# Optimization experiments

Hardware: AMD Instinct MI355X
Metric: run time of the kernel (lower is better)

The kernel has to match this reference:

```python
import jax, jax.numpy as jnp
import numpy as np

DIM = 768
HEADS = 12
HEAD_DIM = DIM // HEADS
SCALE = HEAD_DIM ** -0.5


def setup_inputs() -> dict:
    key = jax.random.key(0)
    ks = jax.random.split(key, 6)
    B, N = 4, 2048
    x = jax.random.normal(ks[0], (B, N, DIM), dtype=jnp.float32)
    s = DIM ** -0.5
    Wq = jax.random.normal(ks[1], (DIM, DIM), dtype=jnp.float32) * s
    Wk = jax.random.normal(ks[2], (DIM, DIM), dtype=jnp.float32) * s
    Wv = jax.random.normal(ks[3], (DIM, DIM), dtype=jnp.float32) * s
    Wp = jax.random.normal(ks[4], (DIM, DIM), dtype=jnp.float32) * s
    bp = jnp.zeros((DIM,), dtype=jnp.float32)
    return {"x": x, "Wq": Wq, "Wk": Wk, "Wv": Wv, "Wp": Wp, "bp": bp}


def reference(x, Wq, Wk, Wv, Wp, bp):
    B, N, C = x.shape
    # separate Q/K/V linears (no bias, qkv_bias=False); torch Linear: x @ W.T
    q = (x @ Wq.T).reshape(B, N, HEADS, HEAD_DIM).transpose(0, 2, 1, 3)
    k = (x @ Wk.T).reshape(B, N, HEADS, HEAD_DIM).transpose(0, 2, 1, 3)
    v = (x @ Wv.T).reshape(B, N, HEADS, HEAD_DIM).transpose(0, 2, 1, 3)
    # explicit full [B,H,N,N] attention matrix, as in the source
    attn = jnp.einsum("bhqd,bhkd->bhqk", q, k) * SCALE
    attn = jax.nn.softmax(attn, axis=-1)
    out = jnp.einsum("bhqk,bhkd->bhqd", attn, v)
    out = out.transpose(0, 2, 1, 3).reshape(B, N, C)
    return out @ Wp.T + bp
```

## Files before the change

kernel.cpp:

```cpp
#include <hip/hip_runtime.h>
#include <cstdint>

#define DIM   768
#define HEADS 12
#define HDIM  64
#define BATCH 4
#define SEQ   2048
#define MROWS (BATCH*SEQ)

typedef __bf16 bf16;
typedef __bf16 bf16x4_t __attribute__((ext_vector_type(4)));
typedef __bf16 bf16x8_t __attribute__((ext_vector_type(8)));
typedef float  f32x4_t  __attribute__((ext_vector_type(4)));
typedef short  short4_t __attribute__((ext_vector_type(4)));

__device__ __forceinline__ f32x4_t mfma16x16x16bf16(bf16x4_t a, bf16x4_t b, f32x4_t c) {
#if __has_builtin(__builtin_amdgcn_mfma_f32_16x16x16_bf16)
    return __builtin_amdgcn_mfma_f32_16x16x16_bf16(a, b, c, 0, 0, 0);
#elif __has_builtin(__builtin_amdgcn_mfma_f32_16x16x16bf16_1k)
    union U { bf16x4_t h; short4_t s; };
    U ua, ub; ua.h = a; ub.h = b;
    return __builtin_amdgcn_mfma_f32_16x16x16bf16_1k(ua.s, ub.s, c, 0, 0, 0);
#else
    asm("v_mfma_f32_16x16x16_bf16 %0, %1, %2, %0" : "+v"(c) : "v"(a), "v"(b));
    return c;
#endif
}

__global__ void cast_bf16_kernel(const float* __restrict__ src, bf16* __restrict__ dst, int n4) {
    int i = blockIdx.x * blockDim.x + threadIdx.x;
    if (i >= n4) return;
    const float4 v = reinterpret_cast<const float4*>(src)[i];
    bf16x4_t o;
    o[0] = (bf16)v.x; o[1] = (bf16)v.y; o[2] = (bf16)v.z; o[3] = (bf16)v.w;
    reinterpret_cast<bf16x4_t*>(dst)[i] = o;
}

__global__ void cast_w4_kernel(const float* __restrict__ s0, const float* __restrict__ s1,
                               const float* __restrict__ s2, const float* __restrict__ s3,
                               bf16* __restrict__ d0, bf16* __restrict__ d1,
                               bf16* __restrict__ d2, bf16* __restrict__ d3, int n4) {
    int i = blockIdx.x * blockDim.x + threadIdx.x;
    if (i >= n4) return;
    int y = blockIdx.y;
    const float* src = (y == 0) ? s0 : (y == 1) ? s1 : (y == 2) ? s2 : s3;
    bf16* dst        = (y == 0) ? d0 : (y == 1) ? d1 : (y == 2) ? d2 : d3;
    const float4 v = reinterpret_cast<const float4*>(src)[i];
    bf16x4_t o;
    o[0] = (bf16)v.x; o[1] = (bf16)v.y; o[2] = (bf16)v.z; o[3] = (bf16)v.w;
    reinterpret_cast<bf16x4_t*>(dst)[i] = o;
}

__device__ __forceinline__ void gload_lds16(const bf16* g, bf16* l) {
    __builtin_amdgcn_global_load_lds((const __attribute__((address_space(1))) void*)g,
                                     (__attribute__((address_space(3))) void*)l, 16, 0, 0);
}

__global__ __launch_bounds__(256, 2) void qkv_gemm(
        const bf16* __restrict__ X,
        const bf16* __restrict__ Wq, const bf16* __restrict__ Wk, const bf16* __restrict__ Wv,
        bf16* __restrict__ Q, bf16* __restrict__ Kd, bf16* __restrict__ Vt)
{
    __shared__ bf16 As[128*32];
    __shared__ bf16 Bs[128*32];
    const int tid  = threadIdx.x;
    const int z    = blockIdx.z;
    const bf16* W  = (z == 0) ? Wq : (z == 1 ? Wk : Wv);
    const int n0   = blockIdx.x * 128;
    const int m0   = blockIdx.y * 128;
    const int lane = tid & 63;
    const int w    = tid >> 6;
    const int wm   = (w & 1) * 64, wn = (w >> 1) * 64;
    const int lr   = lane & 15, quad = lane >> 4;

    f32x4_t acc[4][4] = {};

    for (int kk = 0; kk < DIM; kk += 32) {
        #pragma unroll
        for (int i = 0; i < 2; ++i) {
            int c = tid + i * 256;
            int row = c >> 2, ko = (c & 3) * 8;
            gload_lds16(X + (size_t)(m0 + row) * DIM + kk + ko, &As[row * 32 + ko]);
            gload_lds16(W + (size_t)(n0 + row) * DIM + kk + ko, &Bs[row * 32 + ko]);
        }
        __syncthreads();
        bf16x8_t af[4], bfr[4];
        #pragma unroll
        for (int i = 0; i < 4; ++i)
            af[i] = *reinterpret_cast<const bf16x8_t*>(&As[(wm + i * 16 + lr) * 32 + quad * 8]);
        #pragma unroll
        for (int j = 0; j < 4; ++j)
            bfr[j] = *reinterpret_cast<const bf16x8_t*>(&Bs[(wn + j * 16 + lr) * 32 + quad * 8]);
        #pragma unroll
        for (int i = 0; i < 4; ++i)
            #pragma unroll
            for (int j = 0; j < 4; ++j)
                acc[i][j] = __builtin_amdgcn_mfma_f32_16x16x32_bf16(af[i], bfr[j], acc[i][j], 0, 0, 0);
        __syncthreads();
    }

    #pragma unroll
    for (int i = 0; i < 4; ++i) {
        int mbase = m0 + wm + i * 16 + quad * 4;
        #pragma unroll
        for (int j = 0; j < 4; ++j) {
            int n = n0 + wn + j * 16 + lr;
            int h = n >> 6, d = n & 63;
            #pragma unroll
            for (int r = 0; r < 4; ++r) {
                int m = mbase + r;
                int b = m >> 11, row = m & 2047;
                bf16 v = (bf16)acc[i][j][r];
                if (z < 2) {
                    bf16* dst = (z == 0) ? Q : Kd;
                    dst[(((size_t)b * HEADS + h) * SEQ + row) * HDIM + d] = v;
                } else {
                    Vt[(((size_t)b * HEADS + h) * HDIM + d) * SEQ + row] = v;
                }
            }
        }
    }
}

__global__ __launch_bounds__(256, 2) void out_gemm(
        const bf16* __restrict__ A,
        const bf16* __restrict__ W,
        const float* __restrict__ bias,
        float* __restrict__ out)
{
    __shared__ bf16 As[128*32];
    __shared__ bf16 Bs[128*32];
    const int tid  = threadIdx.x;
    const int n0   = blockIdx.x * 128;
    const int m0   = blockIdx.y * 128;
    const int lane = tid & 63;
    const int w    = tid >> 6;
    const int wm   = (w & 1) * 64, wn = (w >> 1) * 64;
    const int lr   = lane & 15, quad = lane >> 4;

    f32x4_t acc[4][4] = {};

    for (int kk = 0; kk < DIM; kk += 32) {
        #pragma unroll
        for (int i = 0; i < 2; ++i) {
            int c = tid + i * 256;
            int row = c >> 2, ko = (c & 3) * 8;
            gload_lds16(A + (size_t)(m0 + row) * DIM + kk + ko, &As[row * 32 + ko]);
            gload_lds16(W + (size_t)(n0 + row) * DIM + kk + ko, &Bs[row * 32 + ko]);
        }
        __syncthreads();
        bf16x8_t af[4], bfr[4];
        #pragma unroll
        for (int i = 0; i < 4; ++i)
            af[i] = *reinterpret_cast<const bf16x8_t*>(&As[(wm + i * 16 + lr) * 32 + quad * 8]);
        #pragma unroll
        for (int j = 0; j < 4; ++j)
            bfr[j] = *reinterpret_cast<const bf16x8_t*>(&Bs[(wn + j * 16 + lr) * 32 + quad * 8]);
        #pragma unroll
        for (int i = 0; i < 4; ++i)
            #pragma unroll
            for (int j = 0; j < 4; ++j)
                acc[i][j] = __builtin_amdgcn_mfma_f32_16x16x32_bf16(af[i], bfr[j], acc[i][j], 0, 0, 0);
        __syncthreads();
    }

    #pragma unroll
    for (int i = 0; i < 4; ++i) {
        int mbase = m0 + wm + i * 16 + quad * 4;
        #pragma unroll
        for (int j = 0; j < 4; ++j) {
            int n = n0 + wn + j * 16 + lr;
            float bv = bias[n];
            #pragma unroll
            for (int r = 0; r < 4; ++r) {
                int m = mbase + r;
                out[(size_t)m * DIM + n] = acc[i][j][r] + bv;
            }
        }
    }
}

__global__ __launch_bounds__(256, 4) void attn_kernel(
        const bf16* __restrict__ Q, const bf16* __restrict__ Kd,
        const bf16* __restrict__ Vt, bf16* __restrict__ Ab)
{
    __shared__ __align__(16) bf16 KV[2][2][64*64];

    const int tid  = threadIdx.x;
    const int bh   = blockIdx.y;
    const int b    = bh / HEADS, h = bh % HEADS;
    const int q0   = blockIdx.x * 128;
    const int lane = tid & 63, w = tid >> 6;
    const int lr   = lane & 15, quad = lane >> 4;
    const int wq   = w * 32;

    const size_t qkbase = (size_t)bh * SEQ * HDIM;
    const size_t vbase  = (size_t)bh * HDIM * SEQ;

    {
        bf16* Qst = &KV[1][0][0];
        #pragma unroll
        for (int i = 0; i < 4; ++i) {
            int c = tid + i * 256;
            int row = c >> 3, ch = c & 7;
            int gch = ch ^ (row & 7);
            gload_lds16(Q + qkbase + (size_t)(q0 + row) * HDIM + gch * 8, &Qst[row * 64 + ch * 8]);
        }
    }
    auto stageKV = [&](int it, int buf) {
        #pragma unroll
        for (int i = 0; i < 2; ++i) {
            int c = tid + i * 256;
            int row = c >> 3, ch = c & 7;
            int gch = ch ^ (row & 7);
            gload_lds16(Kd + qkbase + (size_t)(it * 64 + row) * HDIM + gch * 8,
                        &KV[buf][0][row * 64 + ch * 8]);
            gload_lds16(Vt + vbase + (size_t)row * SEQ + it * 64 + gch * 8,
                        &KV[buf][1][row * 64 + ch * 8]);
        }
    };
    stageKV(0, 0);
    __syncthreads();

    bf16x8_t qf[2][2];
    {
        const bf16* Qst = &KV[1][0][0];
        #pragma unroll
        for (int q16 = 0; q16 < 2; ++q16) {
            int row = wq + q16 * 16 + lr;
            #pragma unroll
            for (int ks = 0; ks < 2; ++ks) {
                int ch = (ks * 4 + quad) ^ (row & 7);
                qf[q16][ks] = *reinterpret_cast<const bf16x8_t*>(&Qst[row * 64 + ch * 8]);
            }
        }
    }
    __syncthreads();

    f32x4_t oacc[2][4] = {};
    float rs[2] = {0.f, 0.f};
    const float c_scale = 0.18033688011112042f;

    for (int it = 0; it < SEQ / 64; ++it) {
        const int buf = it & 1;
        if (it + 1 < SEQ / 64) stageKV(it + 1, buf ^ 1);

        const bf16* Ks = &KV[buf][0][0];
        const bf16* Vs = &KV[buf][1][0];

        f32x4_t sacc[4][2] = {};
        #pragma unroll
        for (int ks = 0; ks < 2; ++ks) {
            bf16x8_t af[4];
            #pragma unroll
            for (int kt = 0; kt < 4; ++kt) {
                int row = kt * 16 + lr;
                int ch = (ks * 4 + quad) ^ (row & 7);
                af[kt] = *reinterpret_cast<const bf16x8_t*>(&Ks[row * 64 + ch * 8]);
            }
            #pragma unroll
            for (int kt = 0; kt < 4; ++kt)
                #pragma unroll
                for (int q16 = 0; q16 < 2; ++q16)
                    sacc[kt][q16] = __builtin_amdgcn_mfma_f32_16x16x32_bf16(
                        af[kt], qf[q16][ks], sacc[kt][q16], 0, 0, 0);
        }

        #pragma unroll
        for (int kt = 0; kt < 4; ++kt) {
            bf16x4_t bv[4];
            #pragma unroll
            for (int dt = 0; dt < 4; ++dt) {
                int row = dt * 16 + lr;
                int ch = (2 * kt + (quad >> 1)) ^ (row & 7);
                bv[dt] = *reinterpret_cast<const bf16x4_t*>(&Vs[row * 64 + ch * 8 + (quad & 1) * 4]);
            }
            #pragma unroll
            for (int q16 = 0; q16 < 2; ++q16) {
                bf16x4_t pk;
                float s0 = 0.f;
                #pragma unroll
                for (int r = 0; r < 4; ++r) {
                    float p = __builtin_amdgcn_exp2f(sacc[kt][q16][r] * c_scale);
                    s0 += p;
                    pk[r] = (bf16)p;
                }
                rs[q16] += s0;
                #pragma unroll
                for (int dt = 0; dt < 4; ++dt)
                    oacc[q16][dt] = mfma16x16x16bf16(pk, bv[dt], oacc[q16][dt]);
            }
        }
        __syncthreads();
    }

    #pragma unroll
    for (int q16 = 0; q16 < 2; ++q16) {
        rs[q16] += __shfl_xor(rs[q16], 16);
        rs[q16] += __shfl_xor(rs[q16], 32);
    }

    #pragma unroll
    for (int q16 = 0; q16 < 2; ++q16) {
        float inv[4];
        #pragma unroll
        for (int r = 0; r < 4; ++r)
            inv[r] = 1.0f / __shfl(rs[q16], quad * 4 + r);
        #pragma unroll
        for (int dt = 0; dt < 4; ++dt) {
            #pragma unroll
            for (int r = 0; r < 4; ++r) {
                int q = q0 + wq + q16 * 16 + quad * 4 + r;
                Ab[((size_t)b * SEQ + q) * DIM + h * HDIM + dt * 16 + lr] =
                    (bf16)(oacc[q16][dt][r] * inv[r]);
            }
        }
    }
}

extern "C" void kernel_launch(void* const* d_in, const int* in_sizes, int n_in,
                              void* d_out, int out_size, void* d_ws, size_t ws_size,
                              hipStream_t stream) {
    (void)in_sizes; (void)n_in; (void)out_size; (void)ws_size;
    const float* x  = (const float*)d_in[0];
    const float* Wq = (const float*)d_in[1];
    const float* Wk = (const float*)d_in[2];
    const float* Wv = (const float*)d_in[3];
    const float* Wp = (const float*)d_in[4];
    const float* bp = (const float*)d_in[5];
    float* out = (float*)d_out;

    char* ws = (char*)d_ws;
    size_t off = 0;
    auto alloc = [&](size_t bytes) {
        void* p = ws + off;
        off += (bytes + 255) & ~(size_t)255;
        return p;
    };
    const size_t big = (size_t)MROWS * DIM * sizeof(bf16);
    const size_t wsz = (size_t)DIM * DIM * sizeof(bf16);
    bf16* Xb  = (bf16*)alloc(big);
    bf16* Qb  = (bf16*)alloc(big);
    bf16* Kb  = (bf16*)alloc(big);
    bf16* Vtb = (bf16*)alloc(big);
    bf16* Wqb = (bf16*)alloc(wsz);
    bf16* Wkb = (bf16*)alloc(wsz);
    bf16* Wvb = (bf16*)alloc(wsz);
    bf16* Wpb = (bf16*)alloc(wsz);
    bf16* Ab  = Xb;

    const int x4 = MROWS * DIM / 4;
    cast_bf16_kernel<<<(x4 + 255) / 256, 256, 0, stream>>>(x, Xb, x4);
    const int w4 = DIM * DIM / 4;
    cast_w4_kernel<<<dim3((w4 + 255) / 256, 4), 256, 0, stream>>>(
        Wq, Wk, Wv, Wp, Wqb, Wkb, Wvb, Wpb, w4);

    qkv_gemm<<<dim3(DIM / 128, MROWS / 128, 3), 256, 0, stream>>>(Xb, Wqb, Wkb, Wvb, Qb, Kb, Vtb);

    attn_kernel<<<dim3(SEQ / 128, BATCH * HEADS), 256, 0, stream>>>(Qb, Kb, Vtb, Ab);

    out_gemm<<<dim3(DIM / 128, MROWS / 128), 256, 0, stream>>>(Ab, Wpb, bp, out);
}
```

Measured before the change: 252.3 us.

## Compute V transposed via swapped GEMM, fold scale into Q, row sums via MFMA

V is now produced by a separate GEMM that computes Wv·Xᵀ, so the transposed V layout is written with coalesced stores instead of strided scatters. The softmax scale is folded into Q at projection time, and the per-row sum of probabilities is accumulated with an extra MFMA against a ones vector, which removes the scalar adds and cross-lane shuffles. The attention loop also precomputes its staging pointers instead of recomputing addresses each iteration. The trade-offs are an extra kernel launch, one extra MFMA per tile, and row sums accumulated from bf16-rounded probabilities.

```diff
diff --git a/kernel.cpp b/kernel.cpp
--- a/kernel.cpp
+++ b/kernel.cpp
@@ -58,14 +58,14 @@
 
 __global__ __launch_bounds__(256, 2) void qkv_gemm(
         const bf16* __restrict__ X,
-        const bf16* __restrict__ Wq, const bf16* __restrict__ Wk, const bf16* __restrict__ Wv,
-        bf16* __restrict__ Q, bf16* __restrict__ Kd, bf16* __restrict__ Vt)
+        const bf16* __restrict__ Wq, const bf16* __restrict__ Wk,
+        bf16* __restrict__ Q, bf16* __restrict__ Kd)
 {
     __shared__ bf16 As[128*32];
     __shared__ bf16 Bs[128*32];
     const int tid  = threadIdx.x;
     const int z    = blockIdx.z;
-    const bf16* W  = (z == 0) ? Wq : (z == 1 ? Wk : Wv);
+    const bf16* W  = (z == 0) ? Wq : Wk;
     const int n0   = blockIdx.x * 128;
     const int m0   = blockIdx.y * 128;
     const int lane = tid & 63;
@@ -99,6 +99,8 @@
         __syncthreads();
     }
 
+    const float sc = (z == 0) ? 0.18033688011112042f : 1.0f;
+    bf16* dst = (z == 0) ? Q : Kd;
     #pragma unroll
     for (int i = 0; i < 4; ++i) {
         int mbase = m0 + wm + i * 16 + quad * 4;
@@ -110,14 +112,62 @@
             for (int r = 0; r < 4; ++r) {
                 int m = mbase + r;
                 int b = m >> 11, row = m & 2047;
-                bf16 v = (bf16)acc[i][j][r];
-                if (z < 2) {
-                    bf16* dst = (z == 0) ? Q : Kd;
-                    dst[(((size_t)b * HEADS + h) * SEQ + row) * HDIM + d] = v;
-                } else {
-                    Vt[(((size_t)b * HEADS + h) * HDIM + d) * SEQ + row] = v;
-                }
-            }
+                dst[(((size_t)b * HEADS + h) * SEQ + row) * HDIM + d] = (bf16)(acc[i][j][r] * sc);
+            }
+        }
+    }
+}
+
+__global__ __launch_bounds__(256, 2) void vt_gemm(
+        const bf16* __restrict__ Wv,
+        const bf16* __restrict__ X,
+        bf16* __restrict__ Vt)
+{
+    __shared__ bf16 As[128*32];
+    __shared__ bf16 Bs[128*32];
+    const int tid  = threadIdx.x;
+    const int n0   = blockIdx.x * 128;
+    const int m0   = blockIdx.y * 128;
+    const int lane = tid & 63;
+    const int w    = tid >> 6;
+    const int wm   = (w & 1) * 64, wn = (w >> 1) * 64;
+    const int lr   = lane & 15, quad = lane >> 4;
+
+    f32x4_t acc[4][4] = {};
+
+    for (int kk = 0; kk < DIM; kk += 32) {
+        #pragma unroll
+        for (int i = 0; i < 2; ++i) {
+            int c = tid + i * 256;
+            int row = c >> 2, ko = (c & 3) * 8;
+            gload_lds16(Wv + (size_t)(m0 + row) * DIM + kk + ko, &As[row * 32 + ko]);
+            gload_lds16(X  + (size_t)(n0 + row) * DIM + kk + ko, &Bs[row * 32 + ko]);
+        }
+        __syncthreads();
+        bf16x8_t af[4], bfr[4];
+        #pragma unroll
+        for (int i = 0; i < 4; ++i)
+            af[i] = *reinterpret_cast<const bf16x8_t*>(&As[(wm + i * 16 + lr) * 32 + quad * 8]);
+        #pragma unroll
+        for (int j = 0; j < 4; ++j)
+            bfr[j] = *reinterpret_cast<const bf16x8_t*>(&Bs[(wn + j * 16 + lr) * 32 + quad * 8]);
+        #pragma unroll
+        for (int i = 0; i < 4; ++i)
+            #pragma unroll
+            for (int j = 0; j < 4; ++j)
+                acc[i][j] = __builtin_amdgcn_mfma_f32_16x16x32_bf16(af[i], bfr[j], acc[i][j], 0, 0, 0);
+        __syncthreads();
+    }
+
+    #pragma unroll
+    for (int i = 0; i < 4; ++i) {
+        int mbase = m0 + wm + i * 16 + quad * 4;
+        #pragma unroll
+        for (int j = 0; j < 4; ++j) {
+            int n = n0 + wn + j * 16 + lr;
+            #pragma unroll
+            for (int r = 0; r < 4; ++r)
+                Vt[(size_t)(mbase + r) * MROWS + n] = (bf16)acc[i][j][r];
         }
     }
 }
@@ -195,7 +245,12 @@
     const int wq   = w * 32;
 
     const size_t qkbase = (size_t)bh * SEQ * HDIM;
-    const size_t vbase  = (size_t)bh * HDIM * SEQ;
+    const size_t vbase  = (size_t)h * HDIM * MROWS + (size_t)b * SEQ;
+
+    const int src_row = tid >> 3, src_ch = tid & 7;
+    const int src_gch = src_ch ^ (src_row & 7);
+    const int src_row2 = (tid + 256) >> 3, src_ch2 = tid & 7;
+    const int src_gch2 = src_ch2 ^ (src_row2 & 7);
 
     {
         bf16* Qst = &KV[1][0][0];
@@ -207,19 +262,20 @@
             gload_lds16(Q + qkbase + (size_t)(q0 + row) * HDIM + gch * 8, &Qst[row * 64 + ch * 8]);
         }
     }
-    auto stageKV = [&](int it, int buf) {
-        #pragma unroll
-        for (int i = 0; i < 2; ++i) {
-            int c = tid + i * 256;
-            int row = c >> 3, ch = c & 7;
-            int gch = ch ^ (row & 7);
-            gload_lds16(Kd + qkbase + (size_t)(it * 64 + row) * HDIM + gch * 8,
-                        &KV[buf][0][row * 64 + ch * 8]);
-            gload_lds16(Vt + vbase + (size_t)row * SEQ + it * 64 + gch * 8,
-                        &KV[buf][1][row * 64 + ch * 8]);
-        }
-    };
-    stageKV(0, 0);
+
+    const bf16* kp1 = Kd + qkbase + (size_t)src_row  * HDIM + src_gch  * 8;
+    const bf16* kp2 = Kd + qkbase + (size_t)src_row2 * HDIM + src_gch2 * 8;
+    const bf16* vp1 = Vt + vbase  + (size_t)src_row  * MROWS + src_gch  * 8;
+    const bf16* vp2 = Vt + vbase  + (size_t)src_row2 * MROWS + src_gch2 * 8;
+    bf16* kl1 = &KV[0][0][src_row  * 64 + src_ch  * 8];
+    bf16* kl2 = &KV[0][0][src_row2 * 64 + src_ch2 * 8];
+    bf16* vl1 = &KV[0][1][src_row  * 64 + src_ch  * 8];
+    bf16* vl2 = &KV[0][1][src_row2 * 64 + src_ch2 * 8];
+    const ptrdiff_t kstep = 64 * HDIM, vstep = 64;
+    const ptrdiff_t lstep = 2 * 64 * 64;
+
+    gload_lds16(kp1, kl1); gload_lds16(kp2, kl2);
+    gload_lds16(vp1, vl1); gload_lds16(vp2, vl2);
     __syncthreads();
 
     bf16x8_t qf[2][2];
@@ -238,12 +294,18 @@
     __syncthreads();
 
     f32x4_t oacc[2][4] = {};
-    float rs[2] = {0.f, 0.f};
-    const float c_scale = 0.18033688011112042f;
+    f32x4_t rsacc[2] = {};
+    bf16x4_t ones4;
+    ones4[0] = (bf16)1.0f; ones4[1] = (bf16)1.0f; ones4[2] = (bf16)1.0f; ones4[3] = (bf16)1.0f;
 
     for (int it = 0; it < SEQ / 64; ++it) {
         const int buf = it & 1;
-        if (it + 1 < SEQ / 64) stageKV(it + 1, buf ^ 1);
+        if (it + 1 < SEQ / 64) {
+            const ptrdiff_t g = (ptrdiff_t)(it + 1);
+            const ptrdiff_t l = (buf ^ 1) ? lstep : 0;
+            gload_lds16(kp1 + g * kstep, kl1 + l); gload_lds16(kp2 + g * kstep, kl2 + l);
+            gload_lds16(vp1 + g * vstep, vl1 + l); gload_lds16(vp2 + g * vstep, vl2 + l);
+        }
 
         const bf16* Ks = &KV[buf][0][0];
         const bf16* Vs = &KV[buf][1][0];
@@ -278,14 +340,10 @@
             #pragma unroll
             for (int q16 = 0; q16 < 2; ++q16) {
                 bf16x4_t pk;
-                float s0 = 0.f;
                 #pragma unroll
-                for (int r = 0; r < 4; ++r) {
-                    float p = __builtin_amdgcn_exp2f(sacc[kt][q16][r] * c_scale);
-                    s0 += p;
-                    pk[r] = (bf16)p;
-                }
-                rs[q16] += s0;
+                for (int r = 0; r < 4; ++r)
+                    pk[r] = (bf16)__builtin_amdgcn_exp2f(sacc[kt][q16][r]);
+                rsacc[q16] = mfma16x16x16bf16(pk, ones4, rsacc[q16]);
                 #pragma unroll
                 for (int dt = 0; dt < 4; ++dt)
                     oacc[q16][dt] = mfma16x16x16bf16(pk, bv[dt], oacc[q16][dt]);
@@ -296,16 +354,10 @@
 
     #pragma unroll
     for (int q16 = 0; q16 < 2; ++q16) {
-        rs[q16] += __shfl_xor(rs[q16], 16);
-        rs[q16] += __shfl_xor(rs[q16], 32);
-    }
-
-    #pragma unroll
-    for (int q16 = 0; q16 < 2; ++q16) {
         float inv[4];
         #pragma unroll
         for (int r = 0; r < 4; ++r)
-            inv[r] = 1.0f / __shfl(rs[q16], quad * 4 + r);
+            inv[r] = 1.0f / rsacc[q16][r];
         #pragma unroll
         for (int dt = 0; dt < 4; ++dt) {
             #pragma unroll
@@ -355,7 +407,8 @@
     cast_w4_kernel<<<dim3((w4 + 255) / 256, 4), 256, 0, stream>>>(
         Wq, Wk, Wv, Wp, Wqb, Wkb, Wvb, Wpb, w4);
 
-    qkv_gemm<<<dim3(DIM / 128, MROWS / 128, 3), 256, 0, stream>>>(Xb, Wqb, Wkb, Wvb, Qb, Kb, Vtb);
+    qkv_gemm<<<dim3(DIM / 128, MROWS / 128, 2), 256, 0, stream>>>(Xb, Wqb, Wkb, Qb, Kb);
+    vt_gemm<<<dim3(MROWS / 128, DIM / 128), 256, 0, stream>>>(Wvb, Xb, Vtb);
 
     attn_kernel<<<dim3(SEQ / 128, BATCH * HEADS), 256, 0, stream>>>(Qb, Kb, Vtb, Ab);
 
```

New measurement: 234.1 us. -7.2%, faster.
